# Performance work log

Hardware: AMD Instinct MI355X
Metric: run time of the kernel (lower is better)

Reference implementation:

```python
import jax, jax.numpy as jnp
import numpy as np


def setup_inputs() -> dict:
    key = jax.random.key(0)
    distance = jax.random.uniform(key, (16, 2048, 1024), dtype=jnp.float32)
    return {"distance": distance}


def reference(distance):
    # distance: (..., data_length, max_distance)
    original_shape = distance.shape
    L, M = original_shape[-2], original_shape[-1]
    d = distance.reshape(-1, L, M)  # (B, L, M)
    r = jnp.arange(M, dtype=d.dtype)  # range over max_distance

    # weighted mean distance per batch element
    col_sum = d.sum(axis=-2)                                   # (B, M)
    mean_distance = (col_sum * r).sum(axis=-1) / col_sum.sum(axis=-1)  # (B,)
    scales = mean_distance / (0.5 * M)                         # (B,)

    # data-dependent resampling indices along the max_distance axis
    new_idx = (scales[:, None] * r[None, :]).astype(jnp.int32)  # (B, M)
    # TF clips to max_distance (inclusive); gather then reads index M-1 under
    # JAX's clip semantics, which matches clipping to M-1 here.
    new_idx = jnp.clip(new_idx, 0, M - 1)

    idx = jnp.broadcast_to(new_idx[:, None, :], d.shape)        # (B, L, M)
    normed = jnp.take_along_axis(d, idx, axis=-1)               # (B, L, M)
    return normed.reshape(original_shape)
```

## Files before the change

### kernel.cpp

```cpp
#include <hip/hip_runtime.h>


typedef float f32x4 __attribute__((ext_vector_type(4)));

constexpr int L    = 2048;
constexpr int M    = 1024;
constexpr int LCH  = 64;
constexpr int ROWS = L / LCH;
constexpr int RPB  = 8;
constexpr int GPB  = L / RPB;

__global__ __launch_bounds__(256) void colsum_reduce(
    const float* __restrict__ d, double* __restrict__ sums) {
    const int blk = blockIdx.x;
    const int b   = blk / LCH;
    const int lch = blk % LCH;
    const int t   = threadIdx.x;
    const int m0  = t * 4;

    const float* base = d + ((size_t)b * L + (size_t)lch * ROWS) * M + m0;
    float a0 = 0.f, a1 = 0.f, a2 = 0.f, a3 = 0.f;
#pragma unroll 8
    for (int l = 0; l < ROWS; ++l) {
        f32x4 v = *reinterpret_cast<const f32x4*>(base + (size_t)l * M);
        a0 += v.x; a1 += v.y; a2 += v.z; a3 += v.w;
    }
    double s0 = (double)a0 + (double)a1 + (double)a2 + (double)a3;
    double s1 = (double)a0 * (double)(m0 + 0) + (double)a1 * (double)(m0 + 1) +
                (double)a2 * (double)(m0 + 2) + (double)a3 * (double)(m0 + 3);

#pragma unroll
    for (int off = 32; off > 0; off >>= 1) {
        s0 += __shfl_down(s0, off);
        s1 += __shfl_down(s1, off);
    }
    __shared__ double ls0[4], ls1[4];
    const int wave = t >> 6, lane = t & 63;
    if (lane == 0) { ls0[wave] = s0; ls1[wave] = s1; }
    __syncthreads();
    if (t == 0) {
        double S0 = ls0[0] + ls0[1] + ls0[2] + ls0[3];
        double S1 = ls1[0] + ls1[1] + ls1[2] + ls1[3];
        sums[2 * (size_t)blk + 0] = S0;
        sums[2 * (size_t)blk + 1] = S1;
    }
}

__global__ __launch_bounds__(256) void gather_rows(
    const float* __restrict__ d, const double* __restrict__ sums,
    float* __restrict__ out) {
    const int blk = blockIdx.x;
    const int b   = blk / GPB;
    const int l0  = (blk % GPB) * RPB;
    const int t   = threadIdx.x;

    __shared__ float sscale;
    if (t < 64) {
        double s0 = sums[(size_t)b * (2 * LCH) + 2 * t + 0];
        double s1 = sums[(size_t)b * (2 * LCH) + 2 * t + 1];
#pragma unroll
        for (int off = 32; off > 0; off >>= 1) {
            s0 += __shfl_down(s0, off);
            s1 += __shfl_down(s1, off);
        }
        if (t == 0) sscale = (float)((s1 / s0) / (0.5 * (double)M));
    }
    __syncthreads();
    const float sc = sscale;

    const int m0 = t * 4;
    const int i0 = min(max((int)(sc * (float)(m0 + 0)), 0), M - 1);
    const int i1 = min(max((int)(sc * (float)(m0 + 1)), 0), M - 1);
    const int i2 = min(max((int)(sc * (float)(m0 + 2)), 0), M - 1);
    const int i3 = min(max((int)(sc * (float)(m0 + 3)), 0), M - 1);

    const float* rowbase = d   + ((size_t)b * L + l0) * M;
    float*       outbase = out + ((size_t)b * L + l0) * M;
#pragma unroll
    for (int r = 0; r < RPB; ++r) {
        const float* row = rowbase + (size_t)r * M;
        f32x4 v;
        v.x = row[i0];
        v.y = row[i1];
        v.z = row[i2];
        v.w = row[i3];
        __builtin_nontemporal_store(v,
            reinterpret_cast<f32x4*>(outbase + (size_t)r * M + m0));
    }
}

extern "C" void kernel_launch(void* const* d_in, const int* in_sizes, int n_in,
                              void* d_out, int out_size, void* d_ws, size_t ws_size,
                              hipStream_t stream) {
    const float* d = (const float*)d_in[0];
    float* out = (float*)d_out;
    const int n = in_sizes[0];
    const int B = n / (L * M);

    double* sums = (double*)d_ws;

    colsum_reduce<<<B * LCH, 256, 0, stream>>>(d, sums);
    gather_rows<<<B * GPB, 256, 0, stream>>>(d, sums, out);
}
```

Measured before the change: 248.1 us.

## Fuse column-sum and gather into one cooperative kernel with grid sync

Merges the reduction kernel and the gather kernel into a single cooperative launch. Each block first reduces its 32-row chunk, then waits at a grid-wide barrier, then gathers those same rows. The aim is to drop the second kernel launch and to re-read the chunk while it may still sit in cache. The cost is a grid barrier, a requirement that all 1024 blocks be co-resident (hence the occupancy hint in the launch bounds), and fewer, larger blocks in the gather phase.

```diff
diff --git a/kernel.cpp b/kernel.cpp
--- a/kernel.cpp
+++ b/kernel.cpp
@@ -1,63 +1,60 @@
 #include <hip/hip_runtime.h>
+#include <hip/hip_cooperative_groups.h>
+
+namespace cg = cooperative_groups;
 
 
 typedef float f32x4 __attribute__((ext_vector_type(4)));
 
 constexpr int L    = 2048;
 constexpr int M    = 1024;
-constexpr int LCH  = 64;
-constexpr int ROWS = L / LCH;
-constexpr int RPB  = 8;
-constexpr int GPB  = L / RPB;
+constexpr int BPB  = 64;
+constexpr int ROWS = L / BPB;
 
-__global__ __launch_bounds__(256) void colsum_reduce(
-    const float* __restrict__ d, double* __restrict__ sums) {
+__global__ __launch_bounds__(256, 4) void distnorm_fused(
+    const float* __restrict__ d, float* __restrict__ out,
+    double* __restrict__ sums) {
     const int blk = blockIdx.x;
-    const int b   = blk / LCH;
-    const int lch = blk % LCH;
+    const int b   = blk / BPB;
+    const int c   = blk % BPB;
     const int t   = threadIdx.x;
     const int m0  = t * 4;
 
-    const float* base = d + ((size_t)b * L + (size_t)lch * ROWS) * M + m0;
-    float a0 = 0.f, a1 = 0.f, a2 = 0.f, a3 = 0.f;
+    const size_t row0 = ((size_t)b * L + (size_t)c * ROWS) * M;
+
+    {
+        const float* base = d + row0 + m0;
+        float a0 = 0.f, a1 = 0.f, a2 = 0.f, a3 = 0.f;
 #pragma unroll 8
-    for (int l = 0; l < ROWS; ++l) {
-        f32x4 v = *reinterpret_cast<const f32x4*>(base + (size_t)l * M);
-        a0 += v.x; a1 += v.y; a2 += v.z; a3 += v.w;
-    }
-    double s0 = (double)a0 + (double)a1 + (double)a2 + (double)a3;
-    double s1 = (double)a0 * (double)(m0 + 0) + (double)a1 * (double)(m0 + 1) +
-                (double)a2 * (double)(m0 + 2) + (double)a3 * (double)(m0 + 3);
+        for (int l = 0; l < ROWS; ++l) {
+            f32x4 v = *reinterpret_cast<const f32x4*>(base + (size_t)l * M);
+            a0 += v.x; a1 += v.y; a2 += v.z; a3 += v.w;
+        }
+        double s0 = (double)a0 + (double)a1 + (double)a2 + (double)a3;
+        double s1 = (double)a0 * (double)(m0 + 0) + (double)a1 * (double)(m0 + 1) +
+                    (double)a2 * (double)(m0 + 2) + (double)a3 * (double)(m0 + 3);
 
 #pragma unroll
-    for (int off = 32; off > 0; off >>= 1) {
-        s0 += __shfl_down(s0, off);
-        s1 += __shfl_down(s1, off);
+        for (int off = 32; off > 0; off >>= 1) {
+            s0 += __shfl_down(s0, off);
+            s1 += __shfl_down(s1, off);
+        }
+        __shared__ double ls0[4], ls1[4];
+        const int wave = t >> 6, lane = t & 63;
+        if (lane == 0) { ls0[wave] = s0; ls1[wave] = s1; }
+        __syncthreads();
+        if (t == 0) {
+            sums[2 * (size_t)blk + 0] = ls0[0] + ls0[1] + ls0[2] + ls0[3];
+            sums[2 * (size_t)blk + 1] = ls1[0] + ls1[1] + ls1[2] + ls1[3];
+        }
     }
-    __shared__ double ls0[4], ls1[4];
-    const int wave = t >> 6, lane = t & 63;
-    if (lane == 0) { ls0[wave] = s0; ls1[wave] = s1; }
-    __syncthreads();
-    if (t == 0) {
-        double S0 = ls0[0] + ls0[1] + ls0[2] + ls0[3];
-        double S1 = ls1[0] + ls1[1] + ls1[2] + ls1[3];
-        sums[2 * (size_t)blk + 0] = S0;
-        sums[2 * (size_t)blk + 1] = S1;
-    }
-}
 
-__global__ __launch_bounds__(256) void gather_rows(
-    const float* __restrict__ d, const double* __restrict__ sums,
-    float* __restrict__ out) {
-    const int blk = blockIdx.x;
-    const int b   = blk / GPB;
-    const int l0  = (blk % GPB) * RPB;
-    const int t   = threadIdx.x;
+    cg::this_grid().sync();
 
     __shared__ float sscale;
     if (t < 64) {
-        double s0 = sums[(size_t)b * (2 * LCH) + 2 * t + 0];
-        double s1 = sums[(size_t)b * (2 * LCH) + 2 * t + 1];
+        double s0 = sums[(size_t)b * (2 * BPB) + 2 * t + 0];
+        double s1 = sums[(size_t)b * (2 * BPB) + 2 * t + 1];
 #pragma unroll
         for (int off = 32; off > 0; off >>= 1) {
             s0 += __shfl_down(s0, off);
@@ -68,16 +65,15 @@
     __syncthreads();
     const float sc = sscale;
 
-    const int m0 = t * 4;
     const int i0 = min(max((int)(sc * (float)(m0 + 0)), 0), M - 1);
     const int i1 = min(max((int)(sc * (float)(m0 + 1)), 0), M - 1);
     const int i2 = min(max((int)(sc * (float)(m0 + 2)), 0), M - 1);
     const int i3 = min(max((int)(sc * (float)(m0 + 3)), 0), M - 1);
 
-    const float* rowbase = d   + ((size_t)b * L + l0) * M;
-    float*       outbase = out + ((size_t)b * L + l0) * M;
-#pragma unroll
-    for (int r = 0; r < RPB; ++r) {
+    const float* rowbase = d   + row0;
+    float*       outbase = out + row0;
+#pragma unroll 4
+    for (int r = 0; r < ROWS; ++r) {
         const float* row = rowbase + (size_t)r * M;
         f32x4 v;
         v.x = row[i0];
@@ -99,6 +95,7 @@
 
     double* sums = (double*)d_ws;
 
-    colsum_reduce<<<B * LCH, 256, 0, stream>>>(d, sums);
-    gather_rows<<<B * GPB, 256, 0, stream>>>(d, sums, out);
+    void* args[] = {(void*)&d, (void*)&out, (void*)&sums};
+    hipLaunchCooperativeKernel((const void*)distnorm_fused,
+                               dim3(B * BPB), dim3(256), args, 0, stream);
 }
```

Result: slower. 358.6 us (+44.5%).
